# Performance work log

Hardware: AMD Instinct MI355X
Metric: run time of the kernel (lower is better)

## Reference

```python
import jax, jax.numpy as jnp
import numpy as np

K = 1024
HEADS = 16

def setup_inputs() -> dict:
    key = jax.random.key(0)
    ks = jax.random.split(key, 5)
    scale = 0.02
    x = jax.random.normal(ks[0], (2, 2048, K), dtype=jnp.float32)
    Wq = jax.random.normal(ks[1], (K, K), dtype=jnp.float32) * scale
    Wk = jax.random.normal(ks[2], (K, K), dtype=jnp.float32) * scale
    Wv = jax.random.normal(ks[3], (K, K), dtype=jnp.float32) * scale
    Wo = jax.random.normal(ks[4], (K, K), dtype=jnp.float32) * scale
    bo = jnp.zeros((K,), dtype=jnp.float32)
    return {"x": x, "Wq": Wq, "Wk": Wk, "Wv": Wv, "Wo": Wo, "bo": bo}

def reference(x, Wq, Wk, Wv, Wo, bo):
    b, t, k = x.shape
    h = HEADS
    s = k // h
    # projections (torch Linear: x @ W.T; weights here stored as [out,in])
    q = (x @ Wq.T).reshape(b, t, h, s).transpose(0, 2, 1, 3)  # [b,h,t,s]
    kk = (x @ Wk.T).reshape(b, t, h, s).transpose(0, 2, 1, 3)
    v = (x @ Wv.T).reshape(b, t, h, s).transpose(0, 2, 1, 3)
    # NOTE: original scales by sqrt(k) (full model dim), not sqrt(head_dim)
    scores = jnp.einsum('bhts,bhus->bhtu', q, kk) / jnp.sqrt(jnp.float32(k))
    attn = jax.nn.softmax(scores, axis=-1)
    y = jnp.einsum('bhtu,bhus->bhts', attn, v)  # [b,h,t,s]
    y = y.transpose(0, 2, 1, 3).reshape(b, t, k)
    return y @ Wo.T + bo
```

## Files before the change

kernel.cpp:

```cpp
#include <hip/hip_runtime.h>
#include <hip/hip_fp16.h>

typedef _Float16 f16;
typedef __attribute__((ext_vector_type(4))) _Float16 f16x4;
typedef __attribute__((ext_vector_type(8))) _Float16 f16x8;
typedef __attribute__((ext_vector_type(4))) float f32x4;

__device__ __forceinline__ void gload_lds16(const void* g, void* l) {
  __builtin_amdgcn_global_load_lds(
      (const __attribute__((address_space(1))) unsigned*)g,
      (__attribute__((address_space(3))) unsigned*)l, 16, 0, 0);
}

__global__ __launch_bounds__(256) void cvt_kernel(
    const float* __restrict__ x, const float* __restrict__ wq,
    const float* __restrict__ wk, const float* __restrict__ wv,
    const float* __restrict__ wo, f16* __restrict__ xh, f16* __restrict__ wh) {
  const int gid = blockIdx.x * 256 + threadIdx.x;
  const int XV = (4 * 1024 * 1024) / 4;
  if (gid < XV) {
    float4 t = ((const float4*)x)[gid];
    f16x4 o = {(f16)t.x, (f16)t.y, (f16)t.z, (f16)t.w};
    *(f16x4*)&xh[(size_t)gid * 4] = o;
  } else {
    int widx = gid - XV;
    int plane = widx >> 18;
    int off = widx & ((1 << 18) - 1);
    const float* src = (plane == 0) ? wq : (plane == 1) ? wk : (plane == 2) ? wv : wo;
    float4 t = ((const float4*)src)[off];
    if (plane == 0) {
      const float QS = 0.03125f;
      t.x *= QS; t.y *= QS; t.z *= QS; t.w *= QS;
    }
    f16x4 o = {(f16)t.x, (f16)t.y, (f16)t.z, (f16)t.w};
    *(f16x4*)&wh[(size_t)widx * 4] = o;
  }
}

template <int EPI>
__global__ __launch_bounds__(256) void gemm_bt(
    const f16* __restrict__ A, const f16* __restrict__ B, void* __restrict__ Cv,
    const float* __restrict__ bias, int K, int ldc) {
  __shared__ __align__(16) f16 As[128][64];
  __shared__ __align__(16) f16 Bs[128][64];
  const int m0 = blockIdx.y * 128;
  const int n0 = blockIdx.x * 128;
  const int t = threadIdx.x;
  const int w = t >> 6, l = t & 63, g = l >> 4, c = l & 15;
  const int wm = (w >> 1) * 64, wn = (w & 1) * 64;

  f32x4 acc[4][4] = {};
  const int nkt = K >> 6;
  for (int kt = 0; kt < nkt; ++kt) {
#pragma unroll
    for (int i = 0; i < 4; ++i) {
      int ci = i * 256 + w * 64 + l;
      int row = ci >> 3, c8 = ci & 7;
      gload_lds16(&A[(size_t)(m0 + row) * K + kt * 64 + c8 * 8],
                  (char*)&As[0][0] + (i * 256 + w * 64) * 16);
      gload_lds16(&B[(size_t)(n0 + row) * K + kt * 64 + c8 * 8],
                  (char*)&Bs[0][0] + (i * 256 + w * 64) * 16);
    }
    __syncthreads();
#pragma unroll
    for (int kc = 0; kc < 2; ++kc) {
      f16x8 af[4], bf[4];
#pragma unroll
      for (int mi = 0; mi < 4; ++mi)
        af[mi] = *(const f16x8*)&As[wm + mi * 16 + c][(kc * 4 + g) * 8];
#pragma unroll
      for (int ni = 0; ni < 4; ++ni)
        bf[ni] = *(const f16x8*)&Bs[wn + ni * 16 + c][(kc * 4 + g) * 8];
#pragma unroll
      for (int mi = 0; mi < 4; ++mi)
#pragma unroll
        for (int ni = 0; ni < 4; ++ni)
          acc[mi][ni] = __builtin_amdgcn_mfma_f32_16x16x32_f16(af[mi], bf[ni], acc[mi][ni], 0, 0, 0);
    }
    __syncthreads();
  }
#pragma unroll
  for (int mi = 0; mi < 4; ++mi) {
    int rowb = m0 + wm + mi * 16 + 4 * g;
#pragma unroll
    for (int ni = 0; ni < 4; ++ni) {
      int col = n0 + wn + ni * 16 + c;
#pragma unroll
      for (int r = 0; r < 4; ++r) {
        if (EPI == 0) {
          ((f16*)Cv)[(size_t)(rowb + r) * ldc + col] = (f16)acc[mi][ni][r];
        } else {
          ((float*)Cv)[(size_t)(rowb + r) * ldc + col] = acc[mi][ni][r] + bias[col];
        }
      }
    }
  }
}

__global__ __launch_bounds__(256) void attn_kernel(const f16* __restrict__ qkv,
                                                   f16* __restrict__ yh) {
  __shared__ __align__(16) f16 Ks[64][64];
  __shared__ __align__(16) f16 Vt[64][64];
  const int t = threadIdx.x;
  const int w = t >> 6, l = t & 63, g = l >> 4, c = l & 15;
  const int bid = blockIdx.x;
  const int xcd = bid & 7, rest = bid >> 3;
  const int qc = rest & 31, bh = (rest >> 5) * 8 + xcd;
  const int b = bh >> 4, h = bh & 15;
  const int q0 = qc * 64 + w * 16;
  const size_t LD = 3072;
  const f16* qp = qkv + (size_t)(b * 2048) * LD + h * 64;
  const f16* kp = qp + 1024;
  const f16* vp = qp + 2048;

  f16x8 qf[2];
#pragma unroll
  for (int kc = 0; kc < 2; ++kc)
    qf[kc] = *(const f16x8*)&qp[(size_t)(q0 + c) * LD + kc * 32 + g * 8];

  const int rp = t & 31, vd0 = (t >> 5) * 8;

  f32x4 yacc[4] = {};
  float mrow = -1e30f, lrow = 0.f;

  for (int key0 = 0; key0 < 2048; key0 += 64) {
#pragma unroll
    for (int i = 0; i < 2; ++i) {
      int ci = i * 256 + w * 64 + l;
      int row = ci >> 3;
      int c8 = (ci & 7) ^ (row & 7);
      gload_lds16(&kp[(size_t)(key0 + row) * LD + c8 * 8],
                  (char*)&Ks[0][0] + (i * 256 + w * 64) * 16);
    }
    f16x8 va = *(const f16x8*)&vp[(size_t)(key0 + 2 * rp) * LD + vd0];
    f16x8 vb = *(const f16x8*)&vp[(size_t)(key0 + 2 * rp + 1) * LD + vd0];
#pragma unroll
    for (int j = 0; j < 8; ++j) {
      int dd = vd0 + j;
      union { f16 h2[2]; unsigned u; } pk;
      pk.h2[0] = va[j]; pk.h2[1] = vb[j];
      int off = dd * 128 + (((rp >> 2) ^ (dd & 7)) * 16) + 4 * (rp & 3);
      *(unsigned*)((char*)&Vt[0][0] + off) = pk.u;
    }
    __syncthreads();

    f32x4 s[4];
#pragma unroll
    for (int kb = 0; kb < 4; ++kb) {
      f32x4 acc = {};
#pragma unroll
      for (int kc = 0; kc < 2; ++kc) {
        int row = kb * 16 + c;
        f16x8 kf = *(const f16x8*)((char*)&Ks[0][0] + row * 128 +
                                   (((kc * 4 + g) ^ (row & 7)) * 16));
        acc = __builtin_amdgcn_mfma_f32_16x16x32_f16(kf, qf[kc], acc, 0, 0, 0);
      }
      s[kb] = acc;
    }
    float tmax = -1e30f;
#pragma unroll
    for (int kb = 0; kb < 4; ++kb)
#pragma unroll
      for (int r = 0; r < 4; ++r) tmax = fmaxf(tmax, s[kb][r]);
    tmax = fmaxf(tmax, __shfl_xor(tmax, 16, 64));
    tmax = fmaxf(tmax, __shfl_xor(tmax, 32, 64));
    float newm = fmaxf(mrow, tmax);
    float corr = __expf(mrow - newm);
    float psum = 0.f;
    f16x4 pf[4];
#pragma unroll
    for (int kb = 0; kb < 4; ++kb)
#pragma unroll
      for (int r = 0; r < 4; ++r) {
        float p = __expf(s[kb][r] - newm);
        psum += p;
        pf[kb][r] = (f16)p;
      }
    psum += __shfl_xor(psum, 16, 64);
    psum += __shfl_xor(psum, 32, 64);
    lrow = lrow * corr + psum;
    mrow = newm;
#pragma unroll
    for (int sb = 0; sb < 4; ++sb) {
      yacc[sb][0] *= corr; yacc[sb][1] *= corr;
      yacc[sb][2] *= corr; yacc[sb][3] *= corr;
    }
#pragma unroll
    for (int kb = 0; kb < 4; ++kb)
#pragma unroll
      for (int sb = 0; sb < 4; ++sb) {
        int row = sb * 16 + c;
        f16x4 vf = *(const f16x4*)((char*)&Vt[0][0] + row * 128 +
                                   (((2 * kb + (g >> 1)) ^ (row & 7)) * 16) + 8 * (g & 1));
        yacc[sb] = __builtin_amdgcn_mfma_f32_16x16x16f16(vf, pf[kb], yacc[sb], 0, 0, 0);
      }
    __syncthreads();
  }
  const float inv = 1.f / lrow;
#pragma unroll
  for (int sb = 0; sb < 4; ++sb) {
    f16x4 o = {(f16)(yacc[sb][0] * inv), (f16)(yacc[sb][1] * inv),
               (f16)(yacc[sb][2] * inv), (f16)(yacc[sb][3] * inv)};
    *(f16x4*)&yh[(size_t)(b * 2048 + q0 + c) * 1024 + h * 64 + sb * 16 + 4 * g] = o;
  }
}

extern "C" void kernel_launch(void* const* d_in, const int* in_sizes, int n_in,
                              void* d_out, int out_size, void* d_ws, size_t ws_size,
                              hipStream_t stream) {
  (void)in_sizes; (void)n_in; (void)out_size; (void)ws_size;
  const float* x  = (const float*)d_in[0];
  const float* wq = (const float*)d_in[1];
  const float* wk = (const float*)d_in[2];
  const float* wv = (const float*)d_in[3];
  const float* wo = (const float*)d_in[4];
  const float* bo = (const float*)d_in[5];

  f16* xh   = (f16*)d_ws;
  f16* wh   = xh + (size_t)4096 * 1024;
  f16* qkvh = wh + (size_t)4 * 1024 * 1024;
  f16* yh   = qkvh + (size_t)4096 * 3072;
  float* out = (float*)d_out;

  cvt_kernel<<<8192, 256, 0, stream>>>(x, wq, wk, wv, wo, xh, wh);
  gemm_bt<0><<<dim3(24, 32), 256, 0, stream>>>(xh, wh, qkvh, nullptr, 1024, 3072);
  attn_kernel<<<1024, 256, 0, stream>>>(qkvh, yh);
  gemm_bt<1><<<dim3(8, 32), 256, 0, stream>>>(yh, wh + (size_t)3 * 1024 * 1024, out, bo, 1024, 1024);
}
```

Baseline: 231.8 us.

## Double-buffer K/V in attention, process 32 query rows per wave, lazy rescale

The attention kernel now double-buffers the K and V tiles in LDS, prefetching the next key block while computing the current one. Each wave handles two 16-row query blocks, which halves the grid and reuses each K/V fragment across two MFMAs. The softmax switches to exp2 with log2(e) folded into the Q weight scale, and the running max is only rescaled when it grows by more than 8. Register pressure and LDS use increase, and halving the block count may reduce occupancy and CU coverage.

```diff
diff --git a/kernel.cpp b/kernel.cpp
--- a/kernel.cpp
+++ b/kernel.cpp
@@ -29,7 +29,7 @@
     const float* src = (plane == 0) ? wq : (plane == 1) ? wk : (plane == 2) ? wv : wo;
     float4 t = ((const float4*)src)[off];
     if (plane == 0) {
-      const float QS = 0.03125f;
+      const float QS = 0.045084547f;
       t.x *= QS; t.y *= QS; t.z *= QS; t.w *= QS;
     }
     f16x4 o = {(f16)t.x, (f16)t.y, (f16)t.z, (f16)t.w};
@@ -99,109 +99,155 @@
 
 __global__ __launch_bounds__(256) void attn_kernel(const f16* __restrict__ qkv,
                                                    f16* __restrict__ yh) {
-  __shared__ __align__(16) f16 Ks[64][64];
-  __shared__ __align__(16) f16 Vt[64][64];
+  __shared__ __align__(16) f16 Ks[2][64][64];
+  __shared__ __align__(16) f16 Vt[2][64][64];
   const int t = threadIdx.x;
   const int w = t >> 6, l = t & 63, g = l >> 4, c = l & 15;
   const int bid = blockIdx.x;
   const int xcd = bid & 7, rest = bid >> 3;
-  const int qc = rest & 31, bh = (rest >> 5) * 8 + xcd;
+  const int qc = rest & 15, bh = (rest >> 4) * 8 + xcd;
   const int b = bh >> 4, h = bh & 15;
-  const int q0 = qc * 64 + w * 16;
+  const int q0 = qc * 128 + w * 32;
   const size_t LD = 3072;
   const f16* qp = qkv + (size_t)(b * 2048) * LD + h * 64;
   const f16* kp = qp + 1024;
   const f16* vp = qp + 2048;
-
-  f16x8 qf[2];
-#pragma unroll
-  for (int kc = 0; kc < 2; ++kc)
-    qf[kc] = *(const f16x8*)&qp[(size_t)(q0 + c) * LD + kc * 32 + g * 8];
-
   const int rp = t & 31, vd0 = (t >> 5) * 8;
 
-  f32x4 yacc[4] = {};
-  float mrow = -1e30f, lrow = 0.f;
-
-  for (int key0 = 0; key0 < 2048; key0 += 64) {
+  f16x8 qf[2][2];
+#pragma unroll
+  for (int rb = 0; rb < 2; ++rb)
+#pragma unroll
+    for (int kc = 0; kc < 2; ++kc)
+      qf[rb][kc] = *(const f16x8*)&qp[(size_t)(q0 + rb * 16 + c) * LD + kc * 32 + g * 8];
+
+  auto stageK = [&](int buf, int key0) {
 #pragma unroll
     for (int i = 0; i < 2; ++i) {
       int ci = i * 256 + w * 64 + l;
       int row = ci >> 3;
       int c8 = (ci & 7) ^ (row & 7);
       gload_lds16(&kp[(size_t)(key0 + row) * LD + c8 * 8],
-                  (char*)&Ks[0][0] + (i * 256 + w * 64) * 16);
-    }
-    f16x8 va = *(const f16x8*)&vp[(size_t)(key0 + 2 * rp) * LD + vd0];
-    f16x8 vb = *(const f16x8*)&vp[(size_t)(key0 + 2 * rp + 1) * LD + vd0];
+                  (char*)&Ks[buf][0][0] + (i * 256 + w * 64) * 16);
+    }
+  };
+  auto writeV = [&](int buf, f16x8 xa, f16x8 xb) {
 #pragma unroll
     for (int j = 0; j < 8; ++j) {
       int dd = vd0 + j;
       union { f16 h2[2]; unsigned u; } pk;
-      pk.h2[0] = va[j]; pk.h2[1] = vb[j];
+      pk.h2[0] = xa[j]; pk.h2[1] = xb[j];
       int off = dd * 128 + (((rp >> 2) ^ (dd & 7)) * 16) + 4 * (rp & 3);
-      *(unsigned*)((char*)&Vt[0][0] + off) = pk.u;
-    }
-    __syncthreads();
-
-    f32x4 s[4];
+      *(unsigned*)((char*)&Vt[buf][0][0] + off) = pk.u;
+    }
+  };
+
+  f32x4 yacc[2][4] = {};
+  float m[2] = {-1e30f, -1e30f};
+  float lr[2] = {0.f, 0.f};
+
+  stageK(0, 0);
+  {
+    f16x8 va = *(const f16x8*)&vp[(size_t)(2 * rp) * LD + vd0];
+    f16x8 vb = *(const f16x8*)&vp[(size_t)(2 * rp + 1) * LD + vd0];
+    writeV(0, va, vb);
+  }
+  __syncthreads();
+
+  int cur = 0;
+  for (int kt = 0; kt < 32; ++kt) {
+    const bool hn = (kt < 31);
+    f16x8 nva, nvb;
+    if (hn) {
+      int key0n = (kt + 1) * 64;
+      stageK(cur ^ 1, key0n);
+      nva = *(const f16x8*)&vp[(size_t)(key0n + 2 * rp) * LD + vd0];
+      nvb = *(const f16x8*)&vp[(size_t)(key0n + 2 * rp + 1) * LD + vd0];
+    }
+    f32x4 s[2][4];
+    __builtin_amdgcn_s_setprio(1);
 #pragma unroll
     for (int kb = 0; kb < 4; ++kb) {
-      f32x4 acc = {};
-#pragma unroll
-      for (int kc = 0; kc < 2; ++kc) {
-        int row = kb * 16 + c;
-        f16x8 kf = *(const f16x8*)((char*)&Ks[0][0] + row * 128 +
-                                   (((kc * 4 + g) ^ (row & 7)) * 16));
-        acc = __builtin_amdgcn_mfma_f32_16x16x32_f16(kf, qf[kc], acc, 0, 0, 0);
-      }
-      s[kb] = acc;
-    }
-    float tmax = -1e30f;
-#pragma unroll
-    for (int kb = 0; kb < 4; ++kb)
-#pragma unroll
-      for (int r = 0; r < 4; ++r) tmax = fmaxf(tmax, s[kb][r]);
-    tmax = fmaxf(tmax, __shfl_xor(tmax, 16, 64));
-    tmax = fmaxf(tmax, __shfl_xor(tmax, 32, 64));
-    float newm = fmaxf(mrow, tmax);
-    float corr = __expf(mrow - newm);
-    float psum = 0.f;
-    f16x4 pf[4];
-#pragma unroll
-    for (int kb = 0; kb < 4; ++kb)
-#pragma unroll
-      for (int r = 0; r < 4; ++r) {
-        float p = __expf(s[kb][r] - newm);
-        psum += p;
-        pf[kb][r] = (f16)p;
-      }
-    psum += __shfl_xor(psum, 16, 64);
-    psum += __shfl_xor(psum, 32, 64);
-    lrow = lrow * corr + psum;
-    mrow = newm;
-#pragma unroll
-    for (int sb = 0; sb < 4; ++sb) {
-      yacc[sb][0] *= corr; yacc[sb][1] *= corr;
-      yacc[sb][2] *= corr; yacc[sb][3] *= corr;
-    }
+      int row = kb * 16 + c;
+      f16x8 kf0 = *(const f16x8*)((char*)&Ks[cur][0][0] + row * 128 + ((g ^ (row & 7)) * 16));
+      f16x8 kf1 = *(const f16x8*)((char*)&Ks[cur][0][0] + row * 128 + (((4 + g) ^ (row & 7)) * 16));
+#pragma unroll
+      for (int rb = 0; rb < 2; ++rb) {
+        f32x4 acc = {};
+        acc = __builtin_amdgcn_mfma_f32_16x16x32_f16(kf0, qf[rb][0], acc, 0, 0, 0);
+        acc = __builtin_amdgcn_mfma_f32_16x16x32_f16(kf1, qf[rb][1], acc, 0, 0, 0);
+        s[rb][kb] = acc;
+      }
+    }
+    __builtin_amdgcn_s_setprio(0);
+    float pmax[2];
+#pragma unroll
+    for (int rb = 0; rb < 2; ++rb) {
+      float tm = s[rb][0][0];
+#pragma unroll
+      for (int kb = 0; kb < 4; ++kb)
+#pragma unroll
+        for (int r = 0; r < 4; ++r) tm = fmaxf(tm, s[rb][kb][r]);
+      tm = fmaxf(tm, __shfl_xor(tm, 16, 64));
+      tm = fmaxf(tm, __shfl_xor(tm, 32, 64));
+      pmax[rb] = tm;
+    }
+    bool need = (pmax[0] > m[0] + 8.f) || (pmax[1] > m[1] + 8.f);
+    if (__any(need)) {
+#pragma unroll
+      for (int rb = 0; rb < 2; ++rb) {
+        float nm = fmaxf(m[rb], pmax[rb]);
+        float corr = __builtin_amdgcn_exp2f(m[rb] - nm);
+        lr[rb] *= corr;
+#pragma unroll
+        for (int sb = 0; sb < 4; ++sb) {
+          yacc[rb][sb][0] *= corr; yacc[rb][sb][1] *= corr;
+          yacc[rb][sb][2] *= corr; yacc[rb][sb][3] *= corr;
+        }
+        m[rb] = nm;
+      }
+    }
+    f16x4 pf[2][4];
+#pragma unroll
+    for (int rb = 0; rb < 2; ++rb) {
+      float ps = 0.f;
+#pragma unroll
+      for (int kb = 0; kb < 4; ++kb)
+#pragma unroll
+        for (int r = 0; r < 4; ++r) {
+          float p = __builtin_amdgcn_exp2f(s[rb][kb][r] - m[rb]);
+          ps += p;
+          pf[rb][kb][r] = (f16)p;
+        }
+      ps += __shfl_xor(ps, 16, 64);
+      ps += __shfl_xor(ps, 32, 64);
+      lr[rb] += ps;
+    }
+    __builtin_amdgcn_s_setprio(1);
 #pragma unroll
     for (int kb = 0; kb < 4; ++kb)
 #pragma unroll
       for (int sb = 0; sb < 4; ++sb) {
         int row = sb * 16 + c;
-        f16x4 vf = *(const f16x4*)((char*)&Vt[0][0] + row * 128 +
+        f16x4 vf = *(const f16x4*)((char*)&Vt[cur][0][0] + row * 128 +
                                    (((2 * kb + (g >> 1)) ^ (row & 7)) * 16) + 8 * (g & 1));
-        yacc[sb] = __builtin_amdgcn_mfma_f32_16x16x16f16(vf, pf[kb], yacc[sb], 0, 0, 0);
-      }
+        yacc[0][sb] = __builtin_amdgcn_mfma_f32_16x16x16f16(vf, pf[0][kb], yacc[0][sb], 0, 0, 0);
+        yacc[1][sb] = __builtin_amdgcn_mfma_f32_16x16x16f16(vf, pf[1][kb], yacc[1][sb], 0, 0, 0);
+      }
+    __builtin_amdgcn_s_setprio(0);
+    if (hn) writeV(cur ^ 1, nva, nvb);
     __syncthreads();
-  }
-  const float inv = 1.f / lrow;
-#pragma unroll
-  for (int sb = 0; sb < 4; ++sb) {
-    f16x4 o = {(f16)(yacc[sb][0] * inv), (f16)(yacc[sb][1] * inv),
-               (f16)(yacc[sb][2] * inv), (f16)(yacc[sb][3] * inv)};
-    *(f16x4*)&yh[(size_t)(b * 2048 + q0 + c) * 1024 + h * 64 + sb * 16 + 4 * g] = o;
+    cur ^= 1;
+  }
+#pragma unroll
+  for (int rb = 0; rb < 2; ++rb) {
+    float inv = 1.f / lr[rb];
+#pragma unroll
+    for (int sb = 0; sb < 4; ++sb) {
+      f16x4 o = {(f16)(yacc[rb][sb][0] * inv), (f16)(yacc[rb][sb][1] * inv),
+                 (f16)(yacc[rb][sb][2] * inv), (f16)(yacc[rb][sb][3] * inv)};
+      *(f16x4*)&yh[(size_t)(b * 2048 + q0 + rb * 16 + c) * 1024 + h * 64 + sb * 16 + 4 * g] = o;
+    }
   }
 }
 
@@ -224,6 +270,6 @@
 
   cvt_kernel<<<8192, 256, 0, stream>>>(x, wq, wk, wv, wo, xh, wh);
   gemm_bt<0><<<dim3(24, 32), 256, 0, stream>>>(xh, wh, qkvh, nullptr, 1024, 3072);
-  attn_kernel<<<1024, 256, 0, stream>>>(qkvh, yh);
+  attn_kernel<<<512, 256, 0, stream>>>(qkvh, yh);
   gemm_bt<1><<<dim3(8, 32), 256, 0, stream>>>(yh, wh + (size_t)3 * 1024 * 1024, out, bo, 1024, 1024);
 }
```

New measurement: 223.1 us. 1.04x faster.
